# Kernel optimization log

Measured on AMD Instinct MI355X. Metric: run time of the kernel, lower is better.

Reference implementation:

```python
import jax, jax.numpy as jnp
import numpy as np

V, D, N, K, T = 50257, 128, 3, 3, 256
N_STEPS = 5
EPS = 1e-10


def setup_inputs() -> dict:
    key = jax.random.key(0)
    ks = jax.random.split(key, 6)
    tokens = jax.random.randint(ks[0], (T,), 0, V)
    E = jax.random.normal(ks[1], (V, D), dtype=jnp.float32) * 0.02
    # per-foam, per-bubble expression bases (init_spread_foam scale=1.5)
    bases = jax.random.normal(ks[2], (K, N, D, D), dtype=jnp.float32) * (1.5 / np.sqrt(D))
    tension = jax.random.normal(ks[3], (K, N, N), dtype=jnp.float32) * 0.1
    temperature = jnp.ones((K,), jnp.float32)
    target_sim = jnp.zeros((K,), jnp.float32)
    step_size = jnp.full((K,), 0.1, jnp.float32)
    anchor_logit = jnp.zeros((K,), jnp.float32)
    mem_decay_base = jnp.float32(0.8)
    novelty_sens = jnp.float32(1.0)
    return dict(tokens=tokens, E=E, bases=bases, tension=tension,
                temperature=temperature, target_sim=target_sim, step_size=step_size,
                anchor_logit=anchor_logit, mem_decay_base=mem_decay_base,
                novelty_sens=novelty_sens)


def _equilibrate(state, bases, anchor, interaction, target, step, a_w, mask):
    # state: [K,N,D] local coords; bases: [K,N,D,D]; anchor: [K,D]
    anchor_n = anchor / (jnp.linalg.norm(anchor, axis=-1, keepdims=True) + EPS)
    tgt = target[:, None, None]
    for _ in range(N_STEPS):  # fixed small equilibration loop
        expr = jnp.einsum('knd,kned->kne', state, bases)              # [K,N,D]
        expr_n = expr / (jnp.linalg.norm(expr, axis=-1, keepdims=True) + EPS)
        cos = jnp.einsum('kne,kme->knm', expr_n, expr_n)              # [K,N,N]
        fmag = (cos - tgt) * (mask[None] * interaction)               # [K,N,N]
        diff = expr[:, :, None, :] - expr[:, None, :, :]              # [K,N,N,D]
        diff_n = diff / (jnp.linalg.norm(diff, axis=-1, keepdims=True) + EPS)
        forces = jnp.einsum('knm,knmd->knd', fmag, diff_n)            # [K,N,D]
        a_sim = jnp.einsum('kne,ke->kn', expr_n, anchor_n)[..., None] # [K,N,1]
        a_fmag = (a_sim - tgt) * a_w[:, None, None]
        a_diff = expr - anchor[:, None, :]
        a_diff_n = a_diff / (jnp.linalg.norm(a_diff, axis=-1, keepdims=True) + EPS)
        forces = forces + a_fmag * a_diff_n
        f_local = jnp.einsum('kne,kned->knd', forces, bases)
        state = state + step[:, None, None] * f_local
    return state


def reference(tokens, E, bases, tension, temperature, target_sim, step_size,
              anchor_logit, mem_decay_base, novelty_sens):
    mask = 1.0 - jnp.eye(N, dtype=jnp.float32)
    temp = jnp.maximum(jnp.abs(temperature), 0.01)[:, None, None]
    interaction = jax.nn.softmax(-tension / temp, axis=-1)            # [K,N,N]
    step = jnp.clip(jnp.abs(step_size), 0.001, 0.5)
    a_w = jax.nn.sigmoid(anchor_logit)
    sens = jnp.abs(novelty_sens)

    def step_fn(memories, tok):
        x = E[tok]                                                    # [D]
        mem_mean = memories.mean(axis=1)                              # [K,D]
        mem_norm = jnp.linalg.norm(mem_mean, axis=-1) + EPS
        x_norm = jnp.linalg.norm(x) + EPS
        cosv = (mem_mean @ x) / (x_norm * mem_norm)
        novelty = jnp.where(mem_norm > 1e-8, 1.0 - cosv, 1.0)
        decay = jax.nn.sigmoid(mem_decay_base - sens * novelty)       # [K]
        x_wm = x[None, :] + decay[:, None] * mem_mean                 # [K,D]
        state0 = jnp.einsum('ke,kned->knd', x_wm, bases)              # measure into local coords
        state = _equilibrate(state0, bases, x_wm, interaction, target_sim, step, a_w, mask)
        expr = jnp.einsum('knd,kned->kne', state, bases)
        expr_n = expr / (jnp.linalg.norm(expr, axis=-1, keepdims=True) + EPS)
        rho_k = jnp.einsum('kne,knf->kef', expr_n, expr_n) / N        # trace-1 per foam
        memories = decay[:, None, None] * memories + (1.0 - decay)[:, None, None] * state
        rho = rho_k.mean(axis=0)                                      # [D,D]
        eig = jnp.maximum(jnp.linalg.eigvalsh(rho), 1e-12)
        eig = eig / eig.sum()
        logits = jnp.einsum('vd,de,ve->v', E, rho, E)                 # born rule
        probs = jax.nn.softmax(logits)
        S = -(eig * jnp.maximum(jnp.log(eig), -100.0)).sum()
        H = -(probs * jnp.maximum(jnp.log(probs), -100.0)).sum()
        return memories, (probs, S, H, H - S)

    mem0 = jnp.zeros((K, N, D), jnp.float32)
    _, (probs, S, H, F) = jax.lax.scan(step_fn, mem0, tokens)
    return probs, S, H, F
```

## Files before the change

kernel.cpp:

```cpp
#include <hip/hip_runtime.h>
#include <hip/hip_bf16.h>

#define V 50257
#define D 128
#define NN 3
#define KK 3
#define TT 256
#define NSTEPS 5
#define EPSF 1e-10f

#define WS_M  0
#define WS_BT 147456
#define WS_U  294912
#define WS_Z  589824

__device__ __forceinline__ float wred(float v) {
  v += __shfl_xor(v, 1);  v += __shfl_xor(v, 2);  v += __shfl_xor(v, 4);
  v += __shfl_xor(v, 8);  v += __shfl_xor(v, 16); v += __shfl_xor(v, 32);
  return v;
}

__global__ void foam_init(const float* __restrict__ Bg, float* __restrict__ ws)
{
  const int kn = blockIdx.x;
  const int part = blockIdx.y;
  const int tid = threadIdx.x;
  __shared__ float Bs[128][129];
  for (int idx = tid; idx < 16384; idx += 256) {
    int e = idx >> 7, d = idx & 127;
    Bs[e][d] = Bg[(size_t)kn * 16384 + idx];
  }
  __syncthreads();
  float* Mw = ws + WS_M  + (size_t)kn * 16384;
  float* Tw = ws + WS_BT + (size_t)kn * 16384;
  const int base = part * 4096;
  for (int idx = base + tid; idx < base + 4096; idx += 256) {
    int e = idx >> 7, f = idx & 127;
    float acc = 0.f;
    #pragma unroll 4
    for (int d = 0; d < 128; ++d) acc = fmaf(Bs[e][d], Bs[f][d], acc);
    Mw[idx] = acc;
    Tw[idx] = Bs[f][e];
  }
}

__device__ __forceinline__ void matvec3(
  const float (&A0)[32], const float (&A1)[32], const float (&A2)[32],
  const float* v0, const float* v1, const float* v2,
  int f0, float (*parts)[3][132], int r, int c)
{
  float a0 = 0.f, a1 = 0.f, a2 = 0.f;
  #pragma unroll
  for (int j = 0; j < 32; j += 4) {
    const float4 x0 = *reinterpret_cast<const float4*>(v0 + f0 + j);
    const float4 x1 = *reinterpret_cast<const float4*>(v1 + f0 + j);
    const float4 x2 = *reinterpret_cast<const float4*>(v2 + f0 + j);
    a0 = fmaf(A0[j], x0.x, fmaf(A0[j+1], x0.y, fmaf(A0[j+2], x0.z, fmaf(A0[j+3], x0.w, a0))));
    a1 = fmaf(A1[j], x1.x, fmaf(A1[j+1], x1.y, fmaf(A1[j+2], x1.z, fmaf(A1[j+3], x1.w, a1))));
    a2 = fmaf(A2[j], x2.x, fmaf(A2[j+1], x2.y, fmaf(A2[j+2], x2.z, fmaf(A2[j+3], x2.w, a2))));
  }
  parts[c][0][r] = a0; parts[c][1][r] = a1; parts[c][2][r] = a2;
}

__global__ __launch_bounds__(512, 2) void foam_equil(
  const int* __restrict__ tokens, const float* __restrict__ E,
  const float* __restrict__ tension, const float* __restrict__ temperature,
  const float* __restrict__ target_sim, const float* __restrict__ step_size,
  const float* __restrict__ anchor_logit, const float* __restrict__ mdbp,
  const float* __restrict__ sensp, float* __restrict__ ws)
{
  const int k    = blockIdx.x;
  const int tid  = threadIdx.x;
  const int lane = tid & 63;
  const int wv   = tid >> 6;
  const int r    = tid & 127;
  const int c    = tid >> 7;
  const int f0   = c * 32;

  const float* Mw = ws + WS_M  + (size_t)(3 * k) * 16384;
  const float* Tw = ws + WS_BT + (size_t)(3 * k) * 16384;
  float* Uw = ws + WS_U;

  float M0[32], M1[32], M2[32], T0[32], T1[32], T2[32];
  {
    const float* m0 = Mw + r * 128 + f0;
    const float* t0 = Tw + r * 128 + f0;
    #pragma unroll
    for (int j = 0; j < 32; ++j) {
      M0[j] = m0[j];         M1[j] = m0[j + 16384]; M2[j] = m0[j + 32768];
      T0[j] = t0[j];         T1[j] = t0[j + 16384]; T2[j] = t0[j + 32768];
    }
  }

  const float temp = fmaxf(fabsf(temperature[k]), 0.01f);
  const float tgt  = target_sim[k];
  const float stp  = fminf(fmaxf(fabsf(step_size[k]), 0.001f), 0.5f);
  const float aw   = 1.f / (1.f + expf(-anchor_logit[k]));
  const float mdbv = mdbp[0];
  const float sensv = fabsf(sensp[0]);

  __shared__ float inter_s[3][3];
  __shared__ __align__(16) float xs[128], mm[128], xwm[128];
  __shared__ __align__(16) float expr_s[3][128], ffv[3][128], fsv[3][128];
  __shared__ float parts[4][3][132];
  __shared__ float dotb[16];

  if (tid < 9) {
    int n = tid / 3, m = tid % 3;
    float a0 = -tension[(k * 3 + n) * 3 + 0] / temp;
    float a1 = -tension[(k * 3 + n) * 3 + 1] / temp;
    float a2 = -tension[(k * 3 + n) * 3 + 2] / temp;
    float mx = fmaxf(a0, fmaxf(a1, a2));
    float s  = expf(a0 - mx) + expf(a1 - mx) + expf(a2 - mx);
    float av = (m == 0) ? a0 : ((m == 1) ? a1 : a2);
    inter_s[n][m] = expf(av - mx) / s;
  }
  if (tid < 128) mm[tid] = 0.f;
  __syncthreads();

  for (int t = 0; t < TT; ++t) {
    const int tok = tokens[t];
    if (tid < 128) xs[tid] = E[(size_t)tok * 128 + tid];
    {
      int q = tid - 128;
      if (q >= 0) fsv[q >> 7][q & 127] = 0.f;
    }
    __syncthreads();
    if (wv < 3) {
      float p = 0.f;
      for (int f = lane; f < 128; f += 64) {
        float a = (wv == 0) ? xs[f] * xs[f] : ((wv == 1) ? mm[f] * mm[f] : mm[f] * xs[f]);
        p += a;
      }
      p = wred(p);
      if (lane == 0) dotb[wv] = p;
    }
    __syncthreads();
    const float xn   = sqrtf(dotb[0]) + EPSF;
    const float mmn  = sqrtf(dotb[1]) + EPSF;
    const float cosv = dotb[2] / (xn * mmn);
    const float nov  = (mmn > 1e-8f) ? (1.f - cosv) : 1.f;
    const float decay = 1.f / (1.f + expf(-(mdbv - sensv * nov)));
    if (tid < 128) xwm[tid] = xs[tid] + decay * mm[tid];
    __syncthreads();
    matvec3(M0, M1, M2, xwm, xwm, xwm, f0, parts, r, c);
    if (wv == 0) {
      float p = 0.f;
      for (int f = lane; f < 128; f += 64) p += xwm[f] * xwm[f];
      p = wred(p);
      if (lane == 0) dotb[3] = p;
    }
    __syncthreads();
    const float anorm = sqrtf(dotb[3]) + EPSF;
    if (tid < 384) {
      int n = tid >> 7, d = tid & 127;
      expr_s[n][d] = parts[0][n][d] + parts[1][n][d] + parts[2][n][d] + parts[3][n][d];
    }
    __syncthreads();

    for (int it = 0; it < NSTEPS; ++it) {
      for (int dd = wv; dd < 15; dd += 8) {
        float p = 0.f;
        for (int f = lane; f < 128; f += 64) {
          float val;
          if (dd < 3) { float a = expr_s[dd][f]; val = a * a; }
          else if (dd < 6) { int pi = dd - 3; int a = pi >> 1, b = pi ? 2 : 1;
                             val = expr_s[a][f] * expr_s[b][f]; }
          else if (dd < 9) { val = expr_s[dd - 6][f] * xwm[f]; }
          else if (dd < 12) { int pi = dd - 9; int a = pi >> 1, b = pi ? 2 : 1;
                              float dv = expr_s[a][f] - expr_s[b][f]; val = dv * dv; }
          else { float dv = expr_s[dd - 12][f] - xwm[f]; val = dv * dv; }
          p += val;
        }
        p = wred(p);
        if (lane == 0) dotb[dd] = p;
      }
      __syncthreads();
      if (tid < 384) {
        int n = tid >> 7, d = tid & 127;
        float en = sqrtf(dotb[n]) + EPSF;
        float force = 0.f;
        #pragma unroll
        for (int m = 0; m < 3; ++m) {
          if (m == n) continue;
          int pi = n + m - 1;
          float em = sqrtf(dotb[m]) + EPSF;
          float cs = dotb[3 + pi] / (en * em);
          float fmag = (cs - tgt) * inter_s[n][m];
          float dn = sqrtf(dotb[9 + pi]) + EPSF;
          force += fmag * (expr_s[n][d] - expr_s[m][d]) / dn;
        }
        float asim = dotb[6 + n] / (en * anorm);
        float afm = (asim - tgt) * aw;
        float adn = sqrtf(dotb[12 + n]) + EPSF;
        force += afm * (expr_s[n][d] - xwm[d]) / adn;
        ffv[n][d] = force;
        fsv[n][d] += force;
      }
      __syncthreads();
      matvec3(M0, M1, M2, ffv[0], ffv[1], ffv[2], f0, parts, r, c);
      __syncthreads();
      if (tid < 384) {
        int n = tid >> 7, d = tid & 127;
        expr_s[n][d] += stp * (parts[0][n][d] + parts[1][n][d] + parts[2][n][d] + parts[3][n][d]);
      }
      __syncthreads();
    }

    if (tid < 384) {
      int n = tid >> 7, d = tid & 127;
      ffv[n][d] = xwm[d] + stp * fsv[n][d];
    }
    if (wv < 3) {
      float p = 0.f;
      for (int f = lane; f < 128; f += 64) { float a = expr_s[wv][f]; p += a * a; }
      p = wred(p);
      if (lane == 0) dotb[wv] = p;
    }
    __syncthreads();
    matvec3(T0, T1, T2, ffv[0], ffv[1], ffv[2], f0, parts, r, c);
    if (tid < 384) {
      int n = tid >> 7, d = tid & 127;
      float en = sqrtf(dotb[n]) + EPSF;
      Uw[(size_t)t * 1152 + k * 384 + n * 128 + d] = expr_s[n][d] / en;
    }
    __syncthreads();
    if (tid < 128) {
      float sm = 0.f;
      #pragma unroll
      for (int cc = 0; cc < 4; ++cc)
        sm += parts[cc][0][tid] + parts[cc][1][tid] + parts[cc][2][tid];
      sm *= (1.f / 3.f);
      mm[tid] = decay * mm[tid] + (1.f - decay) * sm;
    }
    __syncthreads();
  }
}

__global__ void foam_entropy(const float* __restrict__ U, float* __restrict__ out)
{
  const int t = blockIdx.x;
  const int lane = threadIdx.x;
  __shared__ float Us9[9][132];
  __shared__ float G[9][12];
  for (int idx = lane; idx < 1152; idx += 64)
    Us9[idx >> 7][idx & 127] = U[(size_t)t * 1152 + idx];
  __syncthreads();
  if (lane < 45) {
    int i = 0, rem = lane;
    while (rem >= 9 - i) { rem -= 9 - i; ++i; }
    int j = i + rem;
    float p = 0.f;
    for (int f = 0; f < 128; ++f) p = fmaf(Us9[i][f], Us9[j][f], p);
    p *= (1.f / 9.f);
    G[i][j] = p; G[j][i] = p;
  }
  __syncthreads();
  for (int sw = 0; sw < 8; ++sw) {
    for (int p = 0; p < 8; ++p) {
      for (int q = p + 1; q < 9; ++q) {
        float app = G[p][p], aqq = G[q][q], apq = G[p][q];
        bool doit = fabsf(apq) > 1e-20f;
        float c_ = 1.f, s_ = 0.f;
        if (doit) {
          float tau = (aqq - app) / (2.f * apq);
          float tsg = (tau >= 0.f) ? 1.f : -1.f;
          float tt = tsg / (fabsf(tau) + sqrtf(1.f + tau * tau));
          c_ = 1.f / sqrtf(1.f + tt * tt);
          s_ = tt * c_;
        }
        __syncthreads();
        if (doit) {
          if (lane < 9 && lane != p && lane != q) {
            float gp = G[p][lane], gq = G[q][lane];
            float np_ = c_ * gp - s_ * gq;
            float nq_ = s_ * gp + c_ * gq;
            G[p][lane] = np_; G[lane][p] = np_;
            G[q][lane] = nq_; G[lane][q] = nq_;
          }
          if (lane == 0) {
            float npp = c_ * c_ * app - 2.f * c_ * s_ * apq + s_ * s_ * aqq;
            float nqq = s_ * s_ * app + 2.f * c_ * s_ * apq + c_ * c_ * aqq;
            G[p][p] = npp; G[q][q] = nqq; G[p][q] = 0.f; G[q][p] = 0.f;
          }
        }
        __syncthreads();
      }
    }
  }
  if (lane == 0) {
    float tot = 119.f * 1e-12f;
    float lam[9];
    #pragma unroll
    for (int i = 0; i < 9; ++i) { lam[i] = fmaxf(G[i][i], 1e-12f); tot += lam[i]; }
    float S = 0.f;
    #pragma unroll
    for (int i = 0; i < 9; ++i) {
      float le = lam[i] / tot;
      S -= le * fmaxf(logf(le), -100.f);
    }
    float lz = 1e-12f / tot;
    S -= 119.f * (lz * fmaxf(logf(lz), -100.f));
    out[(size_t)TT * V + t] = S;
  }
}

__global__ __launch_bounds__(256, 2) void foam_logits(
  const float* __restrict__ E, const float* __restrict__ U, float* __restrict__ out)
{
  const int tid = threadIdx.x;
  const int v = blockIdx.x * 256 + tid;
  const bool valid = v < V;
  const int t0 = blockIdx.y * 128;
  float Er[128];
  {
    const float* erow = E + (size_t)(valid ? v : 0) * 128;
    #pragma unroll
    for (int j = 0; j < 128; j += 4) {
      float4 x = *reinterpret_cast<const float4*>(erow + j);
      Er[j] = x.x; Er[j + 1] = x.y; Er[j + 2] = x.z; Er[j + 3] = x.w;
    }
  }
  __shared__ __align__(16) float Us[1152];
  for (int t = t0; t < t0 + 128; ++t) {
    __syncthreads();
    for (int u2 = tid; u2 < 1152; u2 += 256) Us[u2] = U[(size_t)t * 1152 + u2];
    __syncthreads();
    float l = 0.f;
    for (int i = 0; i < 9; ++i) {
      float p = 0.f;
      #pragma unroll
      for (int j = 0; j < 128; j += 4) {
        const float4 uu = *reinterpret_cast<const float4*>(&Us[i * 128 + j]);
        p = fmaf(Er[j], uu.x, fmaf(Er[j + 1], uu.y, fmaf(Er[j + 2], uu.z, fmaf(Er[j + 3], uu.w, p))));
      }
      l = fmaf(p, p, l);
    }
    if (valid) out[(size_t)t * V + v] = l * (1.f / 9.f);
  }
}

__global__ __launch_bounds__(1024) void foam_zh(float* __restrict__ out, float* __restrict__ ws)
{
  const int t = blockIdx.x;
  const int tid = threadIdx.x;
  const float* lg = out + (size_t)t * V;
  float z = 0.f, w = 0.f;
  for (int v = tid; v < V; v += 1024) {
    float l = lg[v];
    float e = expf(l);
    z += e; w = fmaf(l, e, w);
  }
  z = wred(z); w = wred(w);
  __shared__ float zb[16], wb[16];
  if ((tid & 63) == 0) { zb[tid >> 6] = z; wb[tid >> 6] = w; }
  __syncthreads();
  if (tid == 0) {
    float Z = 0.f, W = 0.f;
    #pragma unroll
    for (int i = 0; i < 16; ++i) { Z += zb[i]; W += wb[i]; }
    ws[WS_Z + t] = Z;
    float H = logf(Z) - W / Z;
    out[(size_t)TT * V + TT + t] = H;
    out[(size_t)TT * V + 2 * TT + t] = H - out[(size_t)TT * V + t];
  }
}

__global__ __launch_bounds__(256) void foam_probs(float* __restrict__ out, const float* __restrict__ ws)
{
  const int t = blockIdx.y;
  const int v = blockIdx.x * 256 + threadIdx.x;
  if (v < V) {
    const float zi = 1.f / ws[WS_Z + t];
    float* p = out + (size_t)t * V;
    p[v] = expf(p[v]) * zi;
  }
}

extern "C" void kernel_launch(void* const* d_in, const int* in_sizes, int n_in,
                              void* d_out, int out_size, void* d_ws, size_t ws_size,
                              hipStream_t stream) {
  (void)in_sizes; (void)n_in; (void)out_size; (void)ws_size;
  const int*   tokens      = (const int*)d_in[0];
  const float* E           = (const float*)d_in[1];
  const float* bases       = (const float*)d_in[2];
  const float* tension     = (const float*)d_in[3];
  const float* temperature = (const float*)d_in[4];
  const float* target      = (const float*)d_in[5];
  const float* stepsz      = (const float*)d_in[6];
  const float* alogit      = (const float*)d_in[7];
  const float* mdb         = (const float*)d_in[8];
  const float* sens        = (const float*)d_in[9];
  float* out = (float*)d_out;
  float* ws  = (float*)d_ws;

  foam_init<<<dim3(9, 4), 256, 0, stream>>>(bases, ws);
  foam_equil<<<3, 512, 0, stream>>>(tokens, E, tension, temperature, target,
                                    stepsz, alogit, mdb, sens, ws);
  foam_entropy<<<256, 64, 0, stream>>>(ws + WS_U, out);
  foam_logits<<<dim3(197, 2), 256, 0, stream>>>(E, ws + WS_U, out);
  foam_zh<<<256, 1024, 0, stream>>>(out, ws);
  foam_probs<<<dim3(197, 256), 256, 0, stream>>>(out, ws);
}
```

Measured before the change: 6.096 ms.

## Restructure sequential equilibrium kernel around single-wave Gram reductions and fewer barriers

```diff
diff --git a/kernel.cpp b/kernel.cpp
--- a/kernel.cpp
+++ b/kernel.cpp
@@ -44,25 +44,8 @@
   }
 }
 
-__device__ __forceinline__ void matvec3(
-  const float (&A0)[32], const float (&A1)[32], const float (&A2)[32],
-  const float* v0, const float* v1, const float* v2,
-  int f0, float (*parts)[3][132], int r, int c)
-{
-  float a0 = 0.f, a1 = 0.f, a2 = 0.f;
-  #pragma unroll
-  for (int j = 0; j < 32; j += 4) {
-    const float4 x0 = *reinterpret_cast<const float4*>(v0 + f0 + j);
-    const float4 x1 = *reinterpret_cast<const float4*>(v1 + f0 + j);
-    const float4 x2 = *reinterpret_cast<const float4*>(v2 + f0 + j);
-    a0 = fmaf(A0[j], x0.x, fmaf(A0[j+1], x0.y, fmaf(A0[j+2], x0.z, fmaf(A0[j+3], x0.w, a0))));
-    a1 = fmaf(A1[j], x1.x, fmaf(A1[j+1], x1.y, fmaf(A1[j+2], x1.z, fmaf(A1[j+3], x1.w, a1))));
-    a2 = fmaf(A2[j], x2.x, fmaf(A2[j+1], x2.y, fmaf(A2[j+2], x2.z, fmaf(A2[j+3], x2.w, a2))));
-  }
-  parts[c][0][r] = a0; parts[c][1][r] = a1; parts[c][2][r] = a2;
-}
-
-__global__ __launch_bounds__(512, 2) void foam_equil(
+__global__ __attribute__((amdgpu_flat_work_group_size(512,512), amdgpu_waves_per_eu(2,2)))
+void foam_equil(
   const int* __restrict__ tokens, const float* __restrict__ E,
   const float* __restrict__ tension, const float* __restrict__ temperature,
   const float* __restrict__ target_sim, const float* __restrict__ step_size,
@@ -73,165 +56,223 @@
   const int tid  = threadIdx.x;
   const int lane = tid & 63;
   const int wv   = tid >> 6;
-  const int r    = tid & 127;
-  const int c    = tid >> 7;
-  const int f0   = c * 32;
+  const int fg   = (lane >> 4) & 3;
+  const int dl   = lane & 15;
+  const int down = wv * 16 + dl;
+  const int f0   = fg * 32;
 
   const float* Mw = ws + WS_M  + (size_t)(3 * k) * 16384;
   const float* Tw = ws + WS_BT + (size_t)(3 * k) * 16384;
   float* Uw = ws + WS_U;
 
-  float M0[32], M1[32], M2[32], T0[32], T1[32], T2[32];
-  {
-    const float* m0 = Mw + r * 128 + f0;
-    const float* t0 = Tw + r * 128 + f0;
+  float Mreg[3][32];
+  #pragma unroll
+  for (int n = 0; n < 3; ++n) {
+    const float* src = Mw + n * 16384 + down * 128 + f0;
     #pragma unroll
-    for (int j = 0; j < 32; ++j) {
-      M0[j] = m0[j];         M1[j] = m0[j + 16384]; M2[j] = m0[j + 32768];
-      T0[j] = t0[j];         T1[j] = t0[j + 16384]; T2[j] = t0[j + 32768];
-    }
-  }
-
-  const float temp = fmaxf(fabsf(temperature[k]), 0.01f);
-  const float tgt  = target_sim[k];
-  const float stp  = fminf(fmaxf(fabsf(step_size[k]), 0.001f), 0.5f);
-  const float aw   = 1.f / (1.f + expf(-anchor_logit[k]));
-  const float mdbv = mdbp[0];
+    for (int j = 0; j < 32; ++j) Mreg[n][j] = src[j];
+  }
+
+  const float temp  = fmaxf(fabsf(temperature[k]), 0.01f);
+  const float tgt   = target_sim[k];
+  const float stp   = fminf(fmaxf(fabsf(step_size[k]), 0.001f), 0.5f);
+  const float aw    = 1.f / (1.f + expf(-anchor_logit[k]));
+  const float mdbv  = mdbp[0];
   const float sensv = fabsf(sensp[0]);
 
-  __shared__ float inter_s[3][3];
-  __shared__ __align__(16) float xs[128], mm[128], xwm[128];
-  __shared__ __align__(16) float expr_s[3][128], ffv[3][128], fsv[3][128];
-  __shared__ float parts[4][3][132];
-  __shared__ float dotb[16];
-
-  if (tid < 9) {
-    int n = tid / 3, m = tid % 3;
+  float inter[3][3];
+  #pragma unroll
+  for (int n = 0; n < 3; ++n) {
     float a0 = -tension[(k * 3 + n) * 3 + 0] / temp;
     float a1 = -tension[(k * 3 + n) * 3 + 1] / temp;
     float a2 = -tension[(k * 3 + n) * 3 + 2] / temp;
     float mx = fmaxf(a0, fmaxf(a1, a2));
     float s  = expf(a0 - mx) + expf(a1 - mx) + expf(a2 - mx);
-    float av = (m == 0) ? a0 : ((m == 1) ? a1 : a2);
-    inter_s[n][m] = expf(av - mx) / s;
-  }
-  if (tid < 128) mm[tid] = 0.f;
+    inter[n][0] = expf(a0 - mx) / s;
+    inter[n][1] = expf(a1 - mx) / s;
+    inter[n][2] = expf(a2 - mx) / s;
+  }
+
+  __shared__ __align__(16) float exprL[3][128];
+  __shared__ __align__(16) float fLb[3][128];
+  __shared__ __align__(16) float xwmL[128];
+  __shared__ __align__(16) float mmL[128];
+  __shared__ float scal[2];
+
+  if (tid < 128) mmL[tid] = 0.f;
   __syncthreads();
 
   for (int t = 0; t < TT; ++t) {
-    const int tok = tokens[t];
-    if (tid < 128) xs[tid] = E[(size_t)tok * 128 + tid];
+    float xwA = 0.f, xwB = 0.f, gxx = 0.f, anorm = 0.f, decay = 0.f;
+    float fsA[3], fsB[3];
+
+    if (wv == 0) {
+      const int tok = tokens[t];
+      float xA = E[(size_t)tok * 128 + lane];
+      float xB = E[(size_t)tok * 128 + 64 + lane];
+      float mA = mmL[lane], mB = mmL[lane + 64];
+      float pxx = xA * xA + xB * xB;
+      float pmm = mA * mA + mB * mB;
+      float pmx = mA * xA + mB * xB;
+      pxx = wred(pxx); pmm = wred(pmm); pmx = wred(pmx);
+      float xn   = sqrtf(pxx) + EPSF;
+      float mmn  = sqrtf(pmm) + EPSF;
+      float cosv = pmx / (xn * mmn);
+      float nov  = (mmn > 1e-8f) ? (1.f - cosv) : 1.f;
+      decay = 1.f / (1.f + expf(-(mdbv - sensv * nov)));
+      xwA = xA + decay * mA;
+      xwB = xB + decay * mB;
+      gxx = pxx + 2.f * decay * pmx + decay * decay * pmm;
+      anorm = sqrtf(gxx) + EPSF;
+      xwmL[lane] = xwA; xwmL[lane + 64] = xwB;
+      if (lane == 0) scal[0] = decay;
+      fsA[0] = fsA[1] = fsA[2] = 0.f;
+      fsB[0] = fsB[1] = fsB[2] = 0.f;
+    }
+    __syncthreads();
+
     {
-      int q = tid - 128;
-      if (q >= 0) fsv[q >> 7][q & 127] = 0.f;
-    }
-    __syncthreads();
-    if (wv < 3) {
-      float p = 0.f;
-      for (int f = lane; f < 128; f += 64) {
-        float a = (wv == 0) ? xs[f] * xs[f] : ((wv == 1) ? mm[f] * mm[f] : mm[f] * xs[f]);
-        p += a;
-      }
-      p = wred(p);
-      if (lane == 0) dotb[wv] = p;
-    }
-    __syncthreads();
-    const float xn   = sqrtf(dotb[0]) + EPSF;
-    const float mmn  = sqrtf(dotb[1]) + EPSF;
-    const float cosv = dotb[2] / (xn * mmn);
-    const float nov  = (mmn > 1e-8f) ? (1.f - cosv) : 1.f;
-    const float decay = 1.f / (1.f + expf(-(mdbv - sensv * nov)));
-    if (tid < 128) xwm[tid] = xs[tid] + decay * mm[tid];
-    __syncthreads();
-    matvec3(M0, M1, M2, xwm, xwm, xwm, f0, parts, r, c);
+      float xf[32];
+      const float4* xp = reinterpret_cast<const float4*>(&xwmL[f0]);
+      #pragma unroll
+      for (int jj = 0; jj < 8; ++jj) {
+        float4 x = xp[jj];
+        xf[4*jj] = x.x; xf[4*jj+1] = x.y; xf[4*jj+2] = x.z; xf[4*jj+3] = x.w;
+      }
+      float mv[3];
+      #pragma unroll
+      for (int n = 0; n < 3; ++n) {
+        float a = 0.f;
+        #pragma unroll
+        for (int j = 0; j < 32; ++j) a = fmaf(Mreg[n][j], xf[j], a);
+        a += __shfl_xor(a, 16); a += __shfl_xor(a, 32);
+        mv[n] = a;
+      }
+      if (fg == 0) {
+        exprL[0][down] = mv[0]; exprL[1][down] = mv[1]; exprL[2][down] = mv[2];
+      }
+    }
+    __syncthreads();
+
+    #pragma unroll 1
+    for (int it = 0; it < NSTEPS; ++it) {
+      if (wv == 0) {
+        float eA[3], eB[3];
+        #pragma unroll
+        for (int n = 0; n < 3; ++n) { eA[n] = exprL[n][lane]; eB[n] = exprL[n][lane + 64]; }
+        float g[9];
+        g[0] = eA[0]*eA[0] + eB[0]*eB[0];
+        g[1] = eA[0]*eA[1] + eB[0]*eB[1];
+        g[2] = eA[0]*eA[2] + eB[0]*eB[2];
+        g[3] = eA[1]*eA[1] + eB[1]*eB[1];
+        g[4] = eA[1]*eA[2] + eB[1]*eB[2];
+        g[5] = eA[2]*eA[2] + eB[2]*eB[2];
+        g[6] = eA[0]*xwA + eB[0]*xwB;
+        g[7] = eA[1]*xwA + eB[1]*xwB;
+        g[8] = eA[2]*xwA + eB[2]*xwB;
+        #pragma unroll
+        for (int q = 0; q < 9; ++q) {
+          float vq = g[q];
+          vq += __shfl_xor(vq, 1);  vq += __shfl_xor(vq, 2);  vq += __shfl_xor(vq, 4);
+          vq += __shfl_xor(vq, 8);  vq += __shfl_xor(vq, 16); vq += __shfl_xor(vq, 32);
+          g[q] = vq;
+        }
+        float e0n = sqrtf(g[0]) + EPSF;
+        float e1n = sqrtf(g[3]) + EPSF;
+        float e2n = sqrtf(g[5]) + EPSF;
+        float cq01 = g[1] / (e0n * e1n) - tgt;
+        float cq02 = g[2] / (e0n * e2n) - tgt;
+        float cq12 = g[4] / (e1n * e2n) - tgt;
+        float rd01 = 1.f / (sqrtf(fmaxf(g[0] + g[3] - 2.f * g[1], 0.f)) + EPSF);
+        float rd02 = 1.f / (sqrtf(fmaxf(g[0] + g[5] - 2.f * g[2], 0.f)) + EPSF);
+        float rd12 = 1.f / (sqrtf(fmaxf(g[3] + g[5] - 2.f * g[4], 0.f)) + EPSF);
+        float w01 = cq01 * inter[0][1] * rd01, w10 = cq01 * inter[1][0] * rd01;
+        float w02 = cq02 * inter[0][2] * rd02, w20 = cq02 * inter[2][0] * rd02;
+        float w12 = cq12 * inter[1][2] * rd12, w21 = cq12 * inter[2][1] * rd12;
+        float v0 = (g[6] / (e0n * anorm) - tgt) * aw
+                 / (sqrtf(fmaxf(g[0] + gxx - 2.f * g[6], 0.f)) + EPSF);
+        float v1 = (g[7] / (e1n * anorm) - tgt) * aw
+                 / (sqrtf(fmaxf(g[3] + gxx - 2.f * g[7], 0.f)) + EPSF);
+        float v2 = (g[8] / (e2n * anorm) - tgt) * aw
+                 / (sqrtf(fmaxf(g[5] + gxx - 2.f * g[8], 0.f)) + EPSF);
+        float fA0 = w01*(eA[0]-eA[1]) + w02*(eA[0]-eA[2]) + v0*(eA[0]-xwA);
+        float fA1 = w10*(eA[1]-eA[0]) + w12*(eA[1]-eA[2]) + v1*(eA[1]-xwA);
+        float fA2 = w20*(eA[2]-eA[0]) + w21*(eA[2]-eA[1]) + v2*(eA[2]-xwA);
+        float fB0 = w01*(eB[0]-eB[1]) + w02*(eB[0]-eB[2]) + v0*(eB[0]-xwB);
+        float fB1 = w10*(eB[1]-eB[0]) + w12*(eB[1]-eB[2]) + v1*(eB[1]-xwB);
+        float fB2 = w20*(eB[2]-eB[0]) + w21*(eB[2]-eB[1]) + v2*(eB[2]-xwB);
+        fsA[0] += fA0; fsA[1] += fA1; fsA[2] += fA2;
+        fsB[0] += fB0; fsB[1] += fB1; fsB[2] += fB2;
+        fLb[0][lane] = fA0; fLb[0][lane + 64] = fB0;
+        fLb[1][lane] = fA1; fLb[1][lane + 64] = fB1;
+        fLb[2][lane] = fA2; fLb[2][lane + 64] = fB2;
+      }
+      __syncthreads();
+
+      float mv[3];
+      #pragma unroll
+      for (int n = 0; n < 3; ++n) {
+        const float4* fp = reinterpret_cast<const float4*>(&fLb[n][f0]);
+        float a = 0.f;
+        #pragma unroll
+        for (int jj = 0; jj < 8; ++jj) {
+          float4 x = fp[jj];
+          a = fmaf(Mreg[n][4*jj],   x.x, a);
+          a = fmaf(Mreg[n][4*jj+1], x.y, a);
+          a = fmaf(Mreg[n][4*jj+2], x.z, a);
+          a = fmaf(Mreg[n][4*jj+3], x.w, a);
+        }
+        a += __shfl_xor(a, 16); a += __shfl_xor(a, 32);
+        mv[n] = a;
+      }
+      if (fg == 0) {
+        exprL[0][down] += stp * mv[0];
+        exprL[1][down] += stp * mv[1];
+        exprL[2][down] += stp * mv[2];
+      }
+      __syncthreads();
+    }
+
     if (wv == 0) {
-      float p = 0.f;
-      for (int f = lane; f < 128; f += 64) p += xwm[f] * xwm[f];
-      p = wred(p);
-      if (lane == 0) dotb[3] = p;
-    }
-    __syncthreads();
-    const float anorm = sqrtf(dotb[3]) + EPSF;
-    if (tid < 384) {
-      int n = tid >> 7, d = tid & 127;
-      expr_s[n][d] = parts[0][n][d] + parts[1][n][d] + parts[2][n][d] + parts[3][n][d];
-    }
-    __syncthreads();
-
-    for (int it = 0; it < NSTEPS; ++it) {
-      for (int dd = wv; dd < 15; dd += 8) {
-        float p = 0.f;
-        for (int f = lane; f < 128; f += 64) {
-          float val;
-          if (dd < 3) { float a = expr_s[dd][f]; val = a * a; }
-          else if (dd < 6) { int pi = dd - 3; int a = pi >> 1, b = pi ? 2 : 1;
-                             val = expr_s[a][f] * expr_s[b][f]; }
-          else if (dd < 9) { val = expr_s[dd - 6][f] * xwm[f]; }
-          else if (dd < 12) { int pi = dd - 9; int a = pi >> 1, b = pi ? 2 : 1;
-                              float dv = expr_s[a][f] - expr_s[b][f]; val = dv * dv; }
-          else { float dv = expr_s[dd - 12][f] - xwm[f]; val = dv * dv; }
-          p += val;
+      float eA[3], eB[3];
+      #pragma unroll
+      for (int n = 0; n < 3; ++n) { eA[n] = exprL[n][lane]; eB[n] = exprL[n][lane + 64]; }
+      float s0 = eA[0]*eA[0] + eB[0]*eB[0];
+      float s1 = eA[1]*eA[1] + eB[1]*eB[1];
+      float s2 = eA[2]*eA[2] + eB[2]*eB[2];
+      s0 = wred(s0); s1 = wred(s1); s2 = wred(s2);
+      float r0 = 1.f / (sqrtf(s0) + EPSF);
+      float r1 = 1.f / (sqrtf(s1) + EPSF);
+      float r2 = 1.f / (sqrtf(s2) + EPSF);
+      float* ub = Uw + (size_t)t * 1152 + k * 384;
+      ub[0 * 128 + lane] = eA[0] * r0;  ub[0 * 128 + lane + 64] = eB[0] * r0;
+      ub[1 * 128 + lane] = eA[1] * r1;  ub[1 * 128 + lane + 64] = eB[1] * r1;
+      ub[2 * 128 + lane] = eA[2] * r2;  ub[2 * 128 + lane + 64] = eB[2] * r2;
+      fLb[0][lane] = xwA + stp * fsA[0];  fLb[0][lane + 64] = xwB + stp * fsB[0];
+      fLb[1][lane] = xwA + stp * fsA[1];  fLb[1][lane + 64] = xwB + stp * fsB[1];
+      fLb[2][lane] = xwA + stp * fsA[2];  fLb[2][lane + 64] = xwB + stp * fsB[2];
+    }
+    __syncthreads();
+
+    {
+      float a = 0.f;
+      #pragma unroll
+      for (int n = 0; n < 3; ++n) {
+        const float4* tp = reinterpret_cast<const float4*>(Tw + n * 16384 + down * 128 + f0);
+        const float4* sp = reinterpret_cast<const float4*>(&fLb[n][f0]);
+        #pragma unroll
+        for (int jj = 0; jj < 8; ++jj) {
+          float4 tv = tp[jj];
+          float4 sv = sp[jj];
+          a = fmaf(tv.x, sv.x, a); a = fmaf(tv.y, sv.y, a);
+          a = fmaf(tv.z, sv.z, a); a = fmaf(tv.w, sv.w, a);
         }
-        p = wred(p);
-        if (lane == 0) dotb[dd] = p;
-      }
-      __syncthreads();
-      if (tid < 384) {
-        int n = tid >> 7, d = tid & 127;
-        float en = sqrtf(dotb[n]) + EPSF;
-        float force = 0.f;
-        #pragma unroll
-        for (int m = 0; m < 3; ++m) {
-          if (m == n) continue;
-          int pi = n + m - 1;
-          float em = sqrtf(dotb[m]) + EPSF;
-          float cs = dotb[3 + pi] / (en * em);
-          float fmag = (cs - tgt) * inter_s[n][m];
-          float dn = sqrtf(dotb[9 + pi]) + EPSF;
-          force += fmag * (expr_s[n][d] - expr_s[m][d]) / dn;
-        }
-        float asim = dotb[6 + n] / (en * anorm);
-        float afm = (asim - tgt) * aw;
-        float adn = sqrtf(dotb[12 + n]) + EPSF;
-        force += afm * (expr_s[n][d] - xwm[d]) / adn;
-        ffv[n][d] = force;
-        fsv[n][d] += force;
-      }
-      __syncthreads();
-      matvec3(M0, M1, M2, ffv[0], ffv[1], ffv[2], f0, parts, r, c);
-      __syncthreads();
-      if (tid < 384) {
-        int n = tid >> 7, d = tid & 127;
-        expr_s[n][d] += stp * (parts[0][n][d] + parts[1][n][d] + parts[2][n][d] + parts[3][n][d]);
-      }
-      __syncthreads();
-    }
-
-    if (tid < 384) {
-      int n = tid >> 7, d = tid & 127;
-      ffv[n][d] = xwm[d] + stp * fsv[n][d];
-    }
-    if (wv < 3) {
-      float p = 0.f;
-      for (int f = lane; f < 128; f += 64) { float a = expr_s[wv][f]; p += a * a; }
-      p = wred(p);
-      if (lane == 0) dotb[wv] = p;
-    }
-    __syncthreads();
-    matvec3(T0, T1, T2, ffv[0], ffv[1], ffv[2], f0, parts, r, c);
-    if (tid < 384) {
-      int n = tid >> 7, d = tid & 127;
-      float en = sqrtf(dotb[n]) + EPSF;
-      Uw[(size_t)t * 1152 + k * 384 + n * 128 + d] = expr_s[n][d] / en;
-    }
-    __syncthreads();
-    if (tid < 128) {
-      float sm = 0.f;
-      #pragma unroll
-      for (int cc = 0; cc < 4; ++cc)
-        sm += parts[cc][0][tid] + parts[cc][1][tid] + parts[cc][2][tid];
-      sm *= (1.f / 3.f);
-      mm[tid] = decay * mm[tid] + (1.f - decay) * sm;
+      }
+      a += __shfl_xor(a, 16); a += __shfl_xor(a, 32);
+      if (fg == 0) {
+        float dec = scal[0];
+        mmL[down] = dec * mmL[down] + (1.f - dec) * (a * (1.f / 3.f));
+      }
     }
     __syncthreads();
   }
@@ -311,7 +352,7 @@
   const int tid = threadIdx.x;
   const int v = blockIdx.x * 256 + tid;
   const bool valid = v < V;
-  const int t0 = blockIdx.y * 128;
+  const int t0 = blockIdx.y * 32;
   float Er[128];
   {
     const float* erow = E + (size_t)(valid ? v : 0) * 128;
@@ -322,7 +363,7 @@
     }
   }
   __shared__ __align__(16) float Us[1152];
-  for (int t = t0; t < t0 + 128; ++t) {
+  for (int t = t0; t < t0 + 32; ++t) {
     __syncthreads();
     for (int u2 = tid; u2 < 1152; u2 += 256) Us[u2] = U[(size_t)t * 1152 + u2];
     __syncthreads();
@@ -398,7 +439,7 @@
   foam_equil<<<3, 512, 0, stream>>>(tokens, E, tension, temperature, target,
                                     stepsz, alogit, mdb, sens, ws);
   foam_entropy<<<256, 64, 0, stream>>>(ws + WS_U, out);
-  foam_logits<<<dim3(197, 2), 256, 0, stream>>>(E, ws + WS_U, out);
+  foam_logits<<<dim3(197, 8), 256, 0, stream>>>(E, ws + WS_U, out);
   foam_zh<<<256, 1024, 0, stream>>>(out, ws);
   foam_probs<<<dim3(197, 256), 256, 0, stream>>>(out, ws);
 }
```

Result: faster. 5.711 ms (-6.3%).
